# Kernel optimization log

Hardware: AMD Instinct MI355X
Metric: run time of the kernel (lower is better)

## Reference

```python
import jax, jax.numpy as jnp
import numpy as np

N_FEATS = 128
N_NODES = 100000
N_EDGES = 1000000
NUM_SEGMENTS = 4096


def setup_inputs() -> dict:
    key = jax.random.key(0)
    ks = jax.random.split(key, 10)
    glorot = lambda k, shape: jax.random.uniform(
        k, shape, dtype=jnp.float32,
        minval=-1.0, maxval=1.0) * np.sqrt(6.0 / (shape[0] + shape[1]))
    x_j = jax.random.normal(ks[0], (N_NODES, N_FEATS), dtype=jnp.float32)
    x_i = jax.random.normal(ks[1], (N_NODES, N_FEATS), dtype=jnp.float32)
    edge_index = jax.random.randint(ks[2], (2, N_EDGES), 0, N_NODES)
    edge_index_batch = jnp.sort(jax.random.randint(ks[3], (N_EDGES,), 0, NUM_SEGMENTS))
    w_j = glorot(ks[4], (N_FEATS, N_FEATS))
    w_i = glorot(ks[5], (N_FEATS, N_FEATS))
    bias = jnp.zeros((N_FEATS,), dtype=jnp.float32)
    prelu_w = jnp.array(0.25, dtype=jnp.float32)  # nn.PReLU default init
    # nn.Linear(out_feats, 1) default init: U(-1/sqrt(fan_in), 1/sqrt(fan_in))
    lim = 1.0 / np.sqrt(N_FEATS)
    mlp_W = jax.random.uniform(ks[6], (N_FEATS, 1), dtype=jnp.float32, minval=-lim, maxval=lim)
    mlp_b = jax.random.uniform(ks[7], (1,), dtype=jnp.float32, minval=-lim, maxval=lim)
    return {"x_j": x_j, "x_i": x_i, "edge_index": edge_index,
            "edge_index_batch": edge_index_batch, "w_j": w_j, "w_i": w_i,
            "bias": bias, "prelu_w": prelu_w, "mlp_W": mlp_W, "mlp_b": mlp_b}


def reference(x_j, x_i, edge_index, edge_index_batch, w_j, w_i, bias, prelu_w, mlp_W, mlp_b):
    # project node features: [N, F]
    xi = x_i @ w_i
    xj = x_j @ w_j
    # gather endpoints per edge and fuse bias add: [E, F]
    h = xj[edge_index[0]] + xi[edge_index[1]] + bias
    # PReLU (single shared slope) then Linear(F, 1) -> [E]
    h = jnp.where(h >= 0, h, prelu_w * h)
    alpha = (h @ mlp_W).reshape(-1) + mlp_b[0]
    # per-graph segmented softmax (PyG torch_geometric.utils.softmax)
    seg_max = jax.ops.segment_max(alpha, edge_index_batch, num_segments=NUM_SEGMENTS)
    e = jnp.exp(alpha - seg_max[edge_index_batch])
    seg_sum = jax.ops.segment_sum(e, edge_index_batch, num_segments=NUM_SEGMENTS)
    return e / (seg_sum[edge_index_batch] + 1e-16)
```

## Files before the change

kernel.cpp:

```cpp
#include <hip/hip_runtime.h>
#include <hip/hip_fp16.h>
#include <float.h>

#define NSEG 4096
#define CAP 2048

typedef __attribute__((ext_vector_type(8))) _Float16 half8;
typedef __attribute__((ext_vector_type(4))) float f32x4;

__global__ void seg_bounds(const int* __restrict__ batch, int* __restrict__ segs, int E) {
  int b = blockIdx.x * blockDim.x + threadIdx.x;
  if (b > NSEG) return;
  int lo = 0, hi = E;
  while (lo < hi) { int mid = (lo + hi) >> 1; if (batch[mid] < b) lo = mid + 1; else hi = mid; }
  segs[b] = lo;
}

__global__ __launch_bounds__(256) void pack_w(
    const float* __restrict__ Wj, const float* __restrict__ Wi,
    __half* __restrict__ Wpk) {
  int tid = blockIdx.x * blockDim.x + threadIdx.x;
  for (int idx = tid; idx < 2 * 4 * 8 * 64 * 8; idx += gridDim.x * blockDim.x) {
    int r     = idx & 7;
    int l     = (idx >> 3) & 63;
    int nt    = (idx >> 9) & 7;
    int kt    = (idx >> 12) & 3;
    int which = idx >> 14;
    const float* W = which ? Wi : Wj;
    int k = kt * 32 + (l >> 4) * 8 + r;
    int n = nt * 16 + (l & 15);
    float v = W[k * 128 + n];
    __half hi = __float2half(v);
    __half lo = __float2half(v - __half2float(hi));
    size_t base = ((size_t)which * 32 + (size_t)(kt * 8 + nt)) * 1024;
    Wpk[base + l * 8 + r]       = hi;
    Wpk[base + 512 + l * 8 + r] = lo;
  }
}

__global__ __launch_bounds__(256) void proj_mfma(
    const float* __restrict__ Xj, const float* __restrict__ Xi,
    const float* __restrict__ bias, const __half* __restrict__ Wpk,
    __half* __restrict__ Yj, __half* __restrict__ Yi, int nrows) {
  const int which = blockIdx.y;
  const float* X = which ? Xi : Xj;
  __half* Y = which ? Yi : Yj;
  const _Float16* Wb = (const _Float16*)Wpk + (size_t)which * 32768;

  const int tid  = threadIdx.x;
  const int wid  = tid >> 6;
  const int lane = tid & 63;
  const int lr   = lane & 15;
  const int lg   = lane >> 4;

  const long row0 = (long)blockIdx.x * 128 + wid * 32;

  long rA0 = row0 + lr;
  long rA1 = row0 + 16 + lr;
  const float* pA0 = X + (rA0 < nrows ? rA0 : 0) * 128 + lg * 8;
  const float* pA1 = X + (rA1 < nrows ? rA1 : 0) * 128 + lg * 8;

  float4 av0[4][2], av1[4][2];
  #pragma unroll
  for (int kt = 0; kt < 4; ++kt) {
    av0[kt][0] = *(const float4*)(pA0 + kt * 32);
    av0[kt][1] = *(const float4*)(pA0 + kt * 32 + 4);
    av1[kt][0] = *(const float4*)(pA1 + kt * 32);
    av1[kt][1] = *(const float4*)(pA1 + kt * 32 + 4);
  }

  f32x4 acc[2][8] = {};

#define CVT1(dsth, dstl, idx, val)                                   \
  { float v_ = (val); _Float16 h_ = (_Float16)v_;                    \
    dsth[idx] = h_; dstl[idx] = (_Float16)(v_ - (float)h_); }
#define CVT8(dsth, dstl, v0, v1)                                     \
  CVT1(dsth, dstl, 0, (v0).x) CVT1(dsth, dstl, 1, (v0).y)            \
  CVT1(dsth, dstl, 2, (v0).z) CVT1(dsth, dstl, 3, (v0).w)            \
  CVT1(dsth, dstl, 4, (v1).x) CVT1(dsth, dstl, 5, (v1).y)            \
  CVT1(dsth, dstl, 6, (v1).z) CVT1(dsth, dstl, 7, (v1).w)

  #pragma unroll
  for (int kt = 0; kt < 4; ++kt) {
    half8 a0h, a0l, a1h, a1l;
    CVT8(a0h, a0l, av0[kt][0], av0[kt][1]);
    CVT8(a1h, a1l, av1[kt][0], av1[kt][1]);
    const _Float16* fk = Wb + kt * 8192;
    #pragma unroll
    for (int nt = 0; nt < 8; ++nt) {
      const _Float16* f = fk + nt * 1024 + lane * 8;
      half8 bh = *(const half8*)(f);
      half8 bl = *(const half8*)(f + 512);
      acc[0][nt] = __builtin_amdgcn_mfma_f32_16x16x32_f16(a0h, bh, acc[0][nt], 0, 0, 0);
      acc[1][nt] = __builtin_amdgcn_mfma_f32_16x16x32_f16(a1h, bh, acc[1][nt], 0, 0, 0);
      acc[0][nt] = __builtin_amdgcn_mfma_f32_16x16x32_f16(a0l, bh, acc[0][nt], 0, 0, 0);
      acc[1][nt] = __builtin_amdgcn_mfma_f32_16x16x32_f16(a1l, bh, acc[1][nt], 0, 0, 0);
      acc[0][nt] = __builtin_amdgcn_mfma_f32_16x16x32_f16(a0h, bl, acc[0][nt], 0, 0, 0);
      acc[1][nt] = __builtin_amdgcn_mfma_f32_16x16x32_f16(a1h, bl, acc[1][nt], 0, 0, 0);
    }
  }
#undef CVT8
#undef CVT1

  float bcol[8];
  #pragma unroll
  for (int nt = 0; nt < 8; ++nt) bcol[nt] = which ? bias[nt * 16 + lr] : 0.f;

  #pragma unroll
  for (int mt = 0; mt < 2; ++mt) {
    #pragma unroll
    for (int r = 0; r < 4; ++r) {
      long row = row0 + mt * 16 + lg * 4 + r;
      if (row < nrows) {
        __half* yr = Y + row * 128 + lr;
        #pragma unroll
        for (int nt = 0; nt < 8; ++nt)
          yr[nt * 16] = __float2half(acc[mt][nt][r] + bcol[nt]);
      }
    }
  }
}

__global__ __launch_bounds__(256) void seg_softmax(
    const __half* __restrict__ xjp, const __half* __restrict__ xip,
    const int* __restrict__ ei, const int* __restrict__ segs,
    const float* __restrict__ mlpW, const float* __restrict__ prelu_w,
    const float* __restrict__ mlp_b, float* __restrict__ out, int E) {
  const int start = segs[blockIdx.x];
  const int end = segs[blockIdx.x + 1];
  const int cnt = end - start;
  if (cnt <= 0) return;

  __shared__ float aS[CAP];
  __shared__ float red[8];

  const int tid = threadIdx.x;
  const int lane = tid & 63;
  const int sl = lane & 31;
  const int slot = tid >> 5;
  const int wid = tid >> 6;

  const float4 w = *(const float4*)(mlpW + sl * 4);
  const float pw = prelu_w[0];
  const float mb = mlp_b[0];
  const bool useLds = (cnt <= CAP);

#define GATHER4(node, arr, f01, f23)                                       \
  {                                                                        \
    uint2 u = *(const uint2*)((arr) + (long)(node) * 128 + sl * 4);        \
    f01 = __half22float2(*(__half2*)&u.x);                                 \
    f23 = __half22float2(*(__half2*)&u.y);                                 \
  }

  for (int e = start + slot; e < end; e += 32) {
    int e2 = e + 8, e3 = e + 16, e4 = e + 24;
    bool v2 = (e2 < end), v3 = (e3 < end), v4 = (e4 < end);
    int s1 = ei[e],             d1 = ei[E + e];
    int s2 = v2 ? ei[e2] : s1,  d2 = v2 ? ei[E + e2] : d1;
    int s3 = v3 ? ei[e3] : s1,  d3 = v3 ? ei[E + e3] : d1;
    int s4 = v4 ? ei[e4] : s1,  d4 = v4 ? ei[E + e4] : d1;

    float2 a1lo, a1hi, b1lo, b1hi, a2lo, a2hi, b2lo, b2hi;
    float2 a3lo, a3hi, b3lo, b3hi, a4lo, a4hi, b4lo, b4hi;
    GATHER4(s1, xjp, a1lo, a1hi); GATHER4(d1, xip, b1lo, b1hi);
    GATHER4(s2, xjp, a2lo, a2hi); GATHER4(d2, xip, b2lo, b2hi);
    GATHER4(s3, xjp, a3lo, a3hi); GATHER4(d3, xip, b3lo, b3hi);
    GATHER4(s4, xjp, a4lo, a4hi); GATHER4(d4, xip, b4lo, b4hi);

    float p1, p2, p3, p4;
#define ALPHA(alo, ahi, blo, bhi, p)                                        \
    {                                                                       \
      float h0 = alo.x + blo.x, h1 = alo.y + blo.y;                         \
      float h2 = ahi.x + bhi.x, h3 = ahi.y + bhi.y;                         \
      h0 = h0 >= 0.f ? h0 : pw * h0; h1 = h1 >= 0.f ? h1 : pw * h1;         \
      h2 = h2 >= 0.f ? h2 : pw * h2; h3 = h3 >= 0.f ? h3 : pw * h3;         \
      p = h0 * w.x + h1 * w.y + h2 * w.z + h3 * w.w;                        \
    }
    ALPHA(a1lo, a1hi, b1lo, b1hi, p1);
    ALPHA(a2lo, a2hi, b2lo, b2hi, p2);
    ALPHA(a3lo, a3hi, b3lo, b3hi, p3);
    ALPHA(a4lo, a4hi, b4lo, b4hi, p4);
#undef ALPHA

    #pragma unroll
    for (int off = 1; off < 32; off <<= 1) {
      p1 += __shfl_xor(p1, off, 64);
      p2 += __shfl_xor(p2, off, 64);
      p3 += __shfl_xor(p3, off, 64);
      p4 += __shfl_xor(p4, off, 64);
    }
    if (sl == 0) {
      if (useLds) {
        aS[e - start] = p1 + mb;
        if (v2) aS[e2 - start] = p2 + mb;
        if (v3) aS[e3 - start] = p3 + mb;
        if (v4) aS[e4 - start] = p4 + mb;
      } else {
        out[e] = p1 + mb;
        if (v2) out[e2] = p2 + mb;
        if (v3) out[e3] = p3 + mb;
        if (v4) out[e4] = p4 + mb;
      }
    }
  }
#undef GATHER4
  __syncthreads();

  float m = -FLT_MAX;
  if (useLds) { for (int i = tid; i < cnt; i += 256) m = fmaxf(m, aS[i]); }
  else        { for (int i = tid; i < cnt; i += 256) m = fmaxf(m, out[start + i]); }
  #pragma unroll
  for (int off = 1; off < 64; off <<= 1) m = fmaxf(m, __shfl_xor(m, off, 64));
  if (lane == 0) red[wid] = m;
  __syncthreads();
  m = fmaxf(fmaxf(red[0], red[1]), fmaxf(red[2], red[3]));

  float s = 0.f;
  if (useLds) {
    for (int i = tid; i < cnt; i += 256) { float x = expf(aS[i] - m); aS[i] = x; s += x; }
  } else {
    for (int i = tid; i < cnt; i += 256) { float x = expf(out[start + i] - m); out[start + i] = x; s += x; }
  }
  #pragma unroll
  for (int off = 1; off < 64; off <<= 1) s += __shfl_xor(s, off, 64);
  if (lane == 0) red[4 + wid] = s;
  __syncthreads();
  s = (red[4] + red[5]) + (red[6] + red[7]);

  const float inv = 1.0f / (s + 1e-16f);
  if (useLds) { for (int i = tid; i < cnt; i += 256) out[start + i] = aS[i] * inv; }
  else        { for (int i = tid; i < cnt; i += 256) out[start + i] *= inv; }
}

extern "C" void kernel_launch(void* const* d_in, const int* in_sizes, int n_in,
                              void* d_out, int out_size, void* d_ws, size_t ws_size,
                              hipStream_t stream) {
  const float* x_j      = (const float*)d_in[0];
  const float* x_i      = (const float*)d_in[1];
  const int*   edge_idx = (const int*)d_in[2];
  const int*   batch    = (const int*)d_in[3];
  const float* w_j      = (const float*)d_in[4];
  const float* w_i      = (const float*)d_in[5];
  const float* bias     = (const float*)d_in[6];
  const float* prelu_w  = (const float*)d_in[7];
  const float* mlp_W    = (const float*)d_in[8];
  const float* mlp_b    = (const float*)d_in[9];
  const int nnodes = in_sizes[0] / 128;
  const int E = in_sizes[3];

  __half* Wpk = (__half*)d_ws;
  __half* xjp = Wpk + 65536;
  __half* xip = xjp + (size_t)nnodes * 128;
  int* segs   = (int*)(xip + (size_t)nnodes * 128);

  hipLaunchKernelGGL(seg_bounds, dim3((NSEG + 1 + 255) / 256), dim3(256), 0, stream,
                     batch, segs, E);

  hipLaunchKernelGGL(pack_w, dim3(32), dim3(256), 0, stream, w_j, w_i, Wpk);

  int gblocks = (nnodes + 127) / 128;
  hipLaunchKernelGGL(proj_mfma, dim3(gblocks, 2), dim3(256), 0, stream,
                     x_j, x_i, bias, Wpk, xjp, xip, nnodes);

  hipLaunchKernelGGL(seg_softmax, dim3(NSEG), dim3(256), 0, stream,
                     xjp, xip, edge_idx, segs, mlp_W, prelu_w, mlp_b,
                     (float*)d_out, E);
}
```

Measured before the change: 274.1 us.

## Stage packed weights in LDS, swap MFMA operands for row-contiguous stores, prefetch X

Copies the packed hi/lo fp16 weight tiles for the block's projection into 64KB of shared memory instead of reading them from global memory inside the MFMA loop. It swaps the MFMA operand order so that each lane holds four contiguous output columns of one row, which lets the epilogue write 8-byte packed half stores instead of scattered 2-byte stores. It also software-prefetches the next K-slice of X while the current one is converted. The 64KB LDS footprint limits occupancy, and the projection kernel is only part of the total time alongside the segmented softmax.

```diff
diff --git a/kernel.cpp b/kernel.cpp
--- a/kernel.cpp
+++ b/kernel.cpp
@@ -45,7 +45,8 @@
   const int which = blockIdx.y;
   const float* X = which ? Xi : Xj;
   __half* Y = which ? Yi : Yj;
-  const _Float16* Wb = (const _Float16*)Wpk + (size_t)which * 32768;
+
+  __shared__ _Float16 Wlds[32768];
 
   const int tid  = threadIdx.x;
   const int wid  = tid >> 6;
@@ -53,21 +54,26 @@
   const int lr   = lane & 15;
   const int lg   = lane >> 4;
 
+  {
+    const float4* src = (const float4*)(Wpk + (size_t)which * 32768);
+    float4* dst = (float4*)Wlds;
+    #pragma unroll
+    for (int it = 0; it < 16; ++it)
+      dst[it * 256 + tid] = src[it * 256 + tid];
+  }
+
   const long row0 = (long)blockIdx.x * 128 + wid * 32;
-
-  long rA0 = row0 + lr;
-  long rA1 = row0 + 16 + lr;
-  const float* pA0 = X + (rA0 < nrows ? rA0 : 0) * 128 + lg * 8;
-  const float* pA1 = X + (rA1 < nrows ? rA1 : 0) * 128 + lg * 8;
-
-  float4 av0[4][2], av1[4][2];
-  #pragma unroll
-  for (int kt = 0; kt < 4; ++kt) {
-    av0[kt][0] = *(const float4*)(pA0 + kt * 32);
-    av0[kt][1] = *(const float4*)(pA0 + kt * 32 + 4);
-    av1[kt][0] = *(const float4*)(pA1 + kt * 32);
-    av1[kt][1] = *(const float4*)(pA1 + kt * 32 + 4);
-  }
+  long r0 = row0 + lr;
+  long r1 = row0 + 16 + lr;
+  const float* p0 = X + (r0 < nrows ? r0 : 0) * 128 + lg * 8;
+  const float* p1 = X + (r1 < nrows ? r1 : 0) * 128 + lg * 8;
+
+  float4 xa0 = *(const float4*)(p0);
+  float4 xb0 = *(const float4*)(p0 + 4);
+  float4 xa1 = *(const float4*)(p1);
+  float4 xb1 = *(const float4*)(p1 + 4);
+
+  __syncthreads();
 
   f32x4 acc[2][8] = {};
 
@@ -80,42 +86,62 @@
   CVT1(dsth, dstl, 4, (v1).x) CVT1(dsth, dstl, 5, (v1).y)            \
   CVT1(dsth, dstl, 6, (v1).z) CVT1(dsth, dstl, 7, (v1).w)
 
-  #pragma unroll
-  for (int kt = 0; kt < 4; ++kt) {
-    half8 a0h, a0l, a1h, a1l;
-    CVT8(a0h, a0l, av0[kt][0], av0[kt][1]);
-    CVT8(a1h, a1l, av1[kt][0], av1[kt][1]);
-    const _Float16* fk = Wb + kt * 8192;
-    #pragma unroll
-    for (int nt = 0; nt < 8; ++nt) {
-      const _Float16* f = fk + nt * 1024 + lane * 8;
-      half8 bh = *(const half8*)(f);
-      half8 bl = *(const half8*)(f + 512);
-      acc[0][nt] = __builtin_amdgcn_mfma_f32_16x16x32_f16(a0h, bh, acc[0][nt], 0, 0, 0);
-      acc[1][nt] = __builtin_amdgcn_mfma_f32_16x16x32_f16(a1h, bh, acc[1][nt], 0, 0, 0);
-      acc[0][nt] = __builtin_amdgcn_mfma_f32_16x16x32_f16(a0l, bh, acc[0][nt], 0, 0, 0);
-      acc[1][nt] = __builtin_amdgcn_mfma_f32_16x16x32_f16(a1l, bh, acc[1][nt], 0, 0, 0);
-      acc[0][nt] = __builtin_amdgcn_mfma_f32_16x16x32_f16(a0h, bl, acc[0][nt], 0, 0, 0);
-      acc[1][nt] = __builtin_amdgcn_mfma_f32_16x16x32_f16(a1h, bl, acc[1][nt], 0, 0, 0);
-    }
-  }
+#define MFMA(a, b, c) __builtin_amdgcn_mfma_f32_16x16x32_f16((a), (b), (c), 0, 0, 0)
+
+#define KT_STEP(kt, PREFETCH)                                            \
+  {                                                                      \
+    half8 wh[8], wl[8];                                                  \
+    _Pragma("unroll")                                                    \
+    for (int nt = 0; nt < 8; ++nt) {                                     \
+      const _Float16* f = Wlds + ((kt) * 8 + nt) * 1024 + lane * 8;      \
+      wh[nt] = *(const half8*)(f);                                       \
+      wl[nt] = *(const half8*)(f + 512);                                 \
+    }                                                                    \
+    half8 xh0, xl0, xh1, xl1;                                            \
+    CVT8(xh0, xl0, xa0, xb0);                                            \
+    CVT8(xh1, xl1, xa1, xb1);                                            \
+    if (PREFETCH) {                                                      \
+      xa0 = *(const float4*)(p0 + ((kt) + 1) * 32);                      \
+      xb0 = *(const float4*)(p0 + ((kt) + 1) * 32 + 4);                  \
+      xa1 = *(const float4*)(p1 + ((kt) + 1) * 32);                      \
+      xb1 = *(const float4*)(p1 + ((kt) + 1) * 32 + 4);                  \
+    }                                                                    \
+    _Pragma("unroll")                                                    \
+    for (int nt = 0; nt < 8; ++nt) {                                     \
+      acc[0][nt] = MFMA(wh[nt], xh0, acc[0][nt]);                        \
+      acc[1][nt] = MFMA(wh[nt], xh1, acc[1][nt]);                        \
+      acc[0][nt] = MFMA(wh[nt], xl0, acc[0][nt]);                        \
+      acc[1][nt] = MFMA(wh[nt], xl1, acc[1][nt]);                        \
+      acc[0][nt] = MFMA(wl[nt], xh0, acc[0][nt]);                        \
+      acc[1][nt] = MFMA(wl[nt], xh1, acc[1][nt]);                        \
+    }                                                                    \
+  }
+
+  KT_STEP(0, 1)
+  KT_STEP(1, 1)
+  KT_STEP(2, 1)
+  KT_STEP(3, 0)
+
+#undef KT_STEP
+#undef MFMA
 #undef CVT8
 #undef CVT1
 
-  float bcol[8];
-  #pragma unroll
-  for (int nt = 0; nt < 8; ++nt) bcol[nt] = which ? bias[nt * 16 + lr] : 0.f;
-
   #pragma unroll
   for (int mt = 0; mt < 2; ++mt) {
-    #pragma unroll
-    for (int r = 0; r < 4; ++r) {
-      long row = row0 + mt * 16 + lg * 4 + r;
-      if (row < nrows) {
-        __half* yr = Y + row * 128 + lr;
-        #pragma unroll
-        for (int nt = 0; nt < 8; ++nt)
-          yr[nt * 16] = __float2half(acc[mt][nt][r] + bcol[nt]);
+    long row = row0 + mt * 16 + lr;
+    if (row < nrows) {
+      __half* yr = Y + row * 128;
+      #pragma unroll
+      for (int nt = 0; nt < 8; ++nt) {
+        float4 bv = make_float4(0.f, 0.f, 0.f, 0.f);
+        if (which) bv = *(const float4*)(bias + nt * 16 + lg * 4);
+        __half2 v01 = __floats2half2_rn(acc[mt][nt][0] + bv.x, acc[mt][nt][1] + bv.y);
+        __half2 v23 = __floats2half2_rn(acc[mt][nt][2] + bv.z, acc[mt][nt][3] + bv.w);
+        uint2 u;
+        u.x = *(unsigned int*)&v01;
+        u.y = *(unsigned int*)&v23;
+        *(uint2*)(yr + nt * 16 + lg * 4) = u;
       }
     }
   }
```

Result: faster. 255.9 us (-6.6%).
